# Kernel optimization log

Hardware: AMD Instinct MI355X
Metric: run time of the kernel (lower is better)

The kernel has to match this reference:

```python
import jax, jax.numpy as jnp
import numpy as np

B, P, K, E, H, V, C = 128, 64, 64, 300, 300, 50000, 3


def lstm0(x, Wih, bih, bhh):
    # PyTorch LSTMCell single step with zero initial (h, c) state.
    # gates = x @ Wih^T + bih + Whh @ 0 + bhh ; chunks order: i, f, g, o
    g = x @ Wih.T + bih + bhh
    i, f, gg, o = jnp.split(g, 4, axis=-1)
    c = jax.nn.sigmoid(i) * jnp.tanh(gg)
    return jax.nn.sigmoid(o) * jnp.tanh(c)


def setup_inputs() -> dict:
    key = jax.random.key(0)
    ks = jax.random.split(key, 24)
    d = {}
    d["premise"] = jax.random.randint(ks[0], (B, P), 1, V)
    d["premise_len"] = jax.random.randint(ks[1], (B,), P // 2, P + 1)
    d["hypothesis"] = jax.random.randint(ks[2], (B, K), 1, V)
    d["hypothesis_len"] = jax.random.randint(ks[3], (B,), K // 2, K + 1)
    embed = jax.random.normal(ks[4], (V, E), jnp.float32) * 0.1
    d["embed"] = embed.at[0].set(0.0)  # padding_idx=0
    d["w_e"] = jax.random.uniform(ks[5], (H,), jnp.float32)
    xav = (2.0 / (H + H)) ** 0.5
    d["W_s"] = jax.random.normal(ks[6], (H, H), jnp.float32) * xav
    d["W_t"] = jax.random.normal(ks[7], (H, H), jnp.float32) * xav
    d["W_m"] = jax.random.normal(ks[8], (H, H), jnp.float32) * xav
    d["fc_w"] = jax.random.normal(ks[9], (C, H), jnp.float32) * (2.0 / (H + C)) ** 0.5
    d["fc_b"] = jax.random.uniform(ks[10], (C,), jnp.float32)
    s = 1.0 / np.sqrt(H)
    def cell(k1, k2, k3, k4, in_dim):
        return (jax.random.uniform(k1, (4 * H, in_dim), jnp.float32, -s, s),
                jax.random.uniform(k2, (4 * H, H), jnp.float32, -s, s),
                jax.random.uniform(k3, (4 * H,), jnp.float32, -s, s),
                jax.random.uniform(k4, (4 * H,), jnp.float32, -s, s))
    d["Wih_p"], d["Whh_p"], d["bih_p"], d["bhh_p"] = cell(ks[11], ks[12], ks[13], ks[14], E)
    d["Wih_h"], d["Whh_h"], d["bih_h"], d["bhh_h"] = cell(ks[15], ks[16], ks[17], ks[18], E)
    d["Wih_m"], d["Whh_m"], d["bih_m"], d["bhh_m"] = cell(ks[19], ks[20], ks[21], ks[22], 2 * H)
    return d


def reference(premise, premise_len, hypothesis, hypothesis_len, embed, w_e,
              W_s, W_t, W_m, fc_w, fc_b,
              Wih_p, Whh_p, bih_p, bhh_p,
              Wih_h, Whh_h, bih_h, bhh_h,
              Wih_m, Whh_m, bih_m, bhh_m):
    prem_emb = embed[premise]      # [B,P,E]
    hypo_emb = embed[hypothesis]   # [B,K,E]
    # Original code calls LSTMCell on a whole sequence -> per-token single step
    # with zero initial state (no temporal recurrence in these two cells).
    h_s = lstm0(prem_emb, Wih_p, bih_p, bhh_p)  # [B,P,H]
    h_t = lstm0(hypo_emb, Wih_h, bih_h, bhh_h)  # [B,K,H]
    s_proj = h_s @ W_s.T                         # [B,P,H]
    t_proj = jnp.transpose(h_t @ W_t.T, (1, 0, 2))  # [K,B,H]
    h_t_kb = jnp.transpose(h_t, (1, 0, 2))          # [K,B,H]
    b, p = h_s.shape[0], h_s.shape[1]
    pmask = jnp.arange(p)[None, :] < premise_len[:, None]  # [B,P]
    neg = jnp.finfo(s_proj.dtype).min

    def step(h_m, xs):
        t_k, ht_k = xs  # [B,H], [B,H]
        m_proj = h_m @ W_m.T  # [B,H]
        e = jnp.einsum('bph,h->bp',
                       jnp.tanh(s_proj + t_k[:, None, :] + m_proj[:, None, :]), w_e)
        e = jnp.where(pmask, e, neg)
        alpha = jax.nn.softmax(e, axis=1)           # softmax over valid premise pos
        a = jnp.einsum('bp,bph->bh', alpha, h_s)    # attention-weighted premise
        m = jnp.concatenate([a, ht_k], axis=-1)     # [B,2H]
        # lstm_match is re-invoked with zero state each k in the original
        h_m_new = lstm0(m, Wih_m, bih_m, bhh_m)
        return h_m_new, h_m_new

    _, hs_all = jax.lax.scan(step, jnp.zeros((b, s_proj.shape[-1]), s_proj.dtype),
                             (t_proj, h_t_kb))      # [K,B,H]
    h_fin = hs_all[hypothesis_len - 1, jnp.arange(b)]  # h_m at last valid hypo step
    logits = h_fin @ fc_w.T + fc_b
    return jax.nn.softmax(logits, axis=1)
```

## Files before the change

### kernel.cpp

```cpp
#include <hip/hip_runtime.h>
#include <stdint.h>

typedef unsigned short u16;
typedef __attribute__((ext_vector_type(8))) __bf16 bf16x8;
typedef __attribute__((ext_vector_type(4))) float f32x4;

__device__ __forceinline__ float bf2f(u16 u) {
    union { unsigned int i; float f; } v; v.i = ((unsigned int)u) << 16; return v.f;
}
__device__ __forceinline__ float bf2f_lo(unsigned int u) {
    union { unsigned int i; float f; } v; v.i = u << 16; return v.f;
}
__device__ __forceinline__ float bf2f_hi(unsigned int u) {
    union { unsigned int i; float f; } v; v.i = u & 0xffff0000u; return v.f;
}
__device__ __forceinline__ u16 f2bf(float f) {
    union { float f; unsigned int i; } v; v.f = f;
    unsigned int x = v.i;
    unsigned int r = (x + 0x7fffu + ((x >> 16) & 1u)) >> 16;
    return (u16)r;
}
__device__ __forceinline__ float rdf(const void* p, size_t i, int isbf) {
    return isbf ? bf2f(((const u16*)p)[i]) : ((const float*)p)[i];
}
__device__ __forceinline__ float fast_sigmoid(float x) {
    return __builtin_amdgcn_rcpf(1.f + __expf(-x));
}
__device__ __forceinline__ float fast_tanh(float x) {
    float u = __expf(x + x);
    return 1.f - 2.f * __builtin_amdgcn_rcpf(u + 1.f);
}
__device__ __forceinline__ bf16x8 as_bf8(uint4 u) {
    union { uint4 a; bf16x8 b; } c; c.a = u; return c.b;
}

#define BB 128
#define PP 64
#define KK 64
#define HH 300
#define MROWS 8192
#define KPAD 320
#define N3H 900
#define GLD 912
#define NT1 19
#define NT4 57
#define NW 16

__global__ void detect_dtype(const u16* __restrict__ raw, int* __restrict__ flag) {
    __shared__ int cnt;
    if (threadIdx.x == 0) cnt = 0;
    __syncthreads();
    if (threadIdx.x < 300 && (raw[threadIdx.x] & 0x8000u)) atomicAdd(&cnt, 1);
    __syncthreads();
    if (threadIdx.x == 0) *flag = (cnt < 8) ? 1 : 0;
}

__global__ void pack_w(const void* __restrict__ src, u16* __restrict__ dst,
                       int dstRowsPad, int nsrcRows, int srcld, int colOff, int igo,
                       const int* __restrict__ flag) {
    int i = blockIdx.x * 256 + threadIdx.x;
    if (i >= dstRowsPad * KPAD) return;
    int isbf = *flag;
    int r = i / KPAD, c = i % KPAD;
    u16 v = 0;
    if (r < nsrcRows && c < HH) {
        int sr = igo ? (r < HH ? r : r + HH) : r;
        v = f2bf(rdf(src, (size_t)sr * srcld + colOff + c, isbf));
    }
    dst[i] = v;
}

__global__ void pack_wf(const void* __restrict__ Wm, uint4* __restrict__ dst,
                        const int* __restrict__ flag) {
    int i = blockIdx.x * 256 + threadIdx.x;
    if (i >= NT1 * 10 * 64) return;
    int isbf = *flag;
    int lane = i & 63, ks = (i >> 6) % 10, T = i / 640;
    int j = T * 16 + (lane & 15);
    int k0 = 32 * ks + 8 * (lane >> 4);
    unsigned int d[4];
    #pragma unroll
    for (int q = 0; q < 4; ++q) {
        int ka = k0 + 2 * q, kb = k0 + 2 * q + 1;
        unsigned int lo = (j < 300 && ka < 300) ? f2bf(rdf(Wm, (size_t)j * HH + ka, isbf)) : 0;
        unsigned int hi = (j < 300 && kb < 300) ? f2bf(rdf(Wm, (size_t)j * HH + kb, isbf)) : 0;
        d[q] = lo | (hi << 16);
    }
    uint4 v; v.x = d[0]; v.y = d[1]; v.z = d[2]; v.w = d[3];
    dst[i] = v;
}

__global__ void pack_bias(const void* bip, const void* bhp, const void* bih_, const void* bhh_,
                          const void* bim, const void* bhm,
                          float* bp, float* bh, float* bm, const int* __restrict__ flag) {
    int i = blockIdx.x * 256 + threadIdx.x;
    if (i >= 3 * N3H) return;
    int isbf = *flag;
    int which = i / N3H, r = i % N3H;
    int sr = (r < HH) ? r : r + HH;
    if (which == 0)      bp[r] = rdf(bip, sr, isbf) + rdf(bhp, sr, isbf);
    else if (which == 1) bh[r] = rdf(bih_, sr, isbf) + rdf(bhh_, sr, isbf);
    else                 bm[r] = rdf(bim, sr, isbf) + rdf(bhm, sr, isbf);
}

__global__ void pack_we(const void* __restrict__ we, float* __restrict__ dst,
                        const int* __restrict__ flag) {
    int i = threadIdx.x;
    dst[i] = (i < 300) ? 2.f * rdf(we, i, *flag) : 0.f;
}

__global__ void gather_embed(const int* __restrict__ idx, const void* __restrict__ embed,
                             u16* __restrict__ X, const int* __restrict__ flag) {
    int i = blockIdx.x * 256 + threadIdx.x;
    int isbf = *flag;
    int r = i / KPAD, c = i % KPAD;
    X[i] = (c < HH) ? f2bf(rdf(embed, (size_t)idx[r] * HH + c, isbf)) : (u16)0;
}

__global__ void zero_out(u16* out) { out[threadIdx.x] = 0; }

__global__ __launch_bounds__(256) void gemm_bt(
    const u16* __restrict__ A, const u16* __restrict__ B,
    u16* __restrict__ Cb, const float* __restrict__ bias, int N, int ldc, int frag)
{
    __shared__ __align__(16) u16 At[128 * 32];
    __shared__ __align__(16) u16 Bt[128 * 32];
    const int tid = threadIdx.x;
    const int m0 = blockIdx.x * 128;
    const int n0 = blockIdx.y * 128;
    const int lane = tid & 63;
    const int wave = tid >> 6;
    const int rm = (wave & 1) * 64;
    const int rn = (wave >> 1) * 64;
    const int qr = lane >> 4;
    const int lr = lane & 15;

    f32x4 acc[4][4] = {};

    const int c0 = tid, c1 = tid + 256;
    const int r0 = c0 >> 2, o0 = (c0 & 3) * 8;
    const int r1 = c1 >> 2, o1 = (c1 & 3) * 8;

    for (int k0 = 0; k0 < KPAD; k0 += 32) {
        uint4 a0v = *(const uint4*)(A + (size_t)(m0 + r0) * KPAD + k0 + o0);
        uint4 a1v = *(const uint4*)(A + (size_t)(m0 + r1) * KPAD + k0 + o1);
        uint4 b0v = *(const uint4*)(B + (size_t)(n0 + r0) * KPAD + k0 + o0);
        uint4 b1v = *(const uint4*)(B + (size_t)(n0 + r1) * KPAD + k0 + o1);
        __syncthreads();
        *(uint4*)(At + c0 * 8) = a0v;
        *(uint4*)(At + c1 * 8) = a1v;
        *(uint4*)(Bt + c0 * 8) = b0v;
        *(uint4*)(Bt + c1 * 8) = b1v;
        __syncthreads();
        bf16x8 af[4], bfr[4];
        #pragma unroll
        for (int i = 0; i < 4; ++i) {
            af[i]  = *(const bf16x8*)(At + (rm + i * 16 + lr) * 32 + qr * 8);
            bfr[i] = *(const bf16x8*)(Bt + (rn + i * 16 + lr) * 32 + qr * 8);
        }
        #pragma unroll
        for (int mi = 0; mi < 4; ++mi)
            #pragma unroll
            for (int ni = 0; ni < 4; ++ni)
                acc[mi][ni] = __builtin_amdgcn_mfma_f32_16x16x32_bf16(
                    af[mi], bfr[ni], acc[mi][ni], 0, 0, 0);
    }
    #pragma unroll
    for (int mi = 0; mi < 4; ++mi) {
        #pragma unroll
        for (int ni = 0; ni < 4; ++ni) {
            int n = n0 + rn + ni * 16 + lr;
            int mb = m0 + rm + mi * 16 + qr * 4;
            if (!frag) {
                if (n >= ldc) continue;
                if (n < N) {
                    float bv = bias ? bias[n] : 0.f;
                    #pragma unroll
                    for (int r = 0; r < 4; ++r)
                        Cb[(size_t)(mb + r) * ldc + n] = f2bf(acc[mi][ni][r] + bv);
                } else {
                    #pragma unroll
                    for (int r = 0; r < 4; ++r)
                        Cb[(size_t)(mb + r) * ldc + n] = 0;
                }
            } else {
                if (n >= GLD) continue;
                int bb = mb >> 6, p0 = mb & 63;
                size_t base = ((((size_t)bb * NT4 + (n >> 4)) * 2 + (p0 >> 5)) * 64
                               + ((p0 >> 3) & 3) * 16 + (n & 15)) * 8 + (p0 & 7);
                u16 wv[4];
                if (n < N) {
                    float bv = bias ? bias[n] : 0.f;
                    #pragma unroll
                    for (int r = 0; r < 4; ++r) wv[r] = f2bf(acc[mi][ni][r] + bv);
                } else {
                    #pragma unroll
                    for (int r = 0; r < 4; ++r) wv[r] = 0;
                }
                uint2 st;
                st.x = (unsigned int)wv[0] | ((unsigned int)wv[1] << 16);
                st.y = (unsigned int)wv[2] | ((unsigned int)wv[3] << 16);
                *(uint2*)(Cb + base) = st;
            }
        }
    }
}

__global__ void lstm_act(const u16* __restrict__ gates, u16* __restrict__ hout) {
    int idx = blockIdx.x * 256 + threadIdx.x;
    int r = idx / KPAD, c = idx % KPAD;
    float h = 0.f;
    if (c < HH) {
        const u16* g = gates + (size_t)r * N3H;
        float gi = bf2f(g[c]);
        float gg = bf2f(g[c + HH]);
        float go = bf2f(g[c + 2 * HH]);
        float cc = fast_sigmoid(gi) * fast_tanh(gg);
        h = fast_sigmoid(go) * fast_tanh(cc);
    }
    hout[idx] = f2bf(h);
}

__global__ __launch_bounds__(1024)
__attribute__((amdgpu_waves_per_eu(4, 4)))
void scan_kernel(
    const u16* __restrict__ sproj,
    const u16* __restrict__ tproj,
    const uint4* __restrict__ Gmf,
    const u16* __restrict__ hp,
    const uint4* __restrict__ Wf,
    const float* __restrict__ we2g,
    const int* __restrict__ premise_len,
    const int* __restrict__ hypothesis_len,
    float* __restrict__ hfin)
{
    __shared__ __align__(16) uint4 gml[NT4 * 2 * 64];
    __shared__ __align__(16) uint4 wlds[3 * 10 * 64];
    __shared__ __align__(16) float tpm[320];
    __shared__ __align__(16) unsigned int hmhi[160];
    __shared__ __align__(16) unsigned int hmlo[160];
    __shared__ __align__(16) float part[NW][64];
    __shared__ __align__(16) u16 aw_sh[128];
    __shared__ __align__(16) float gates[912];

    const int b = blockIdx.x, t = threadIdx.x;
    const int lane = t & 63, w = t >> 6;
    const int lr = lane & 15, qr = lane >> 4;
    const int plen = premise_len[b], hlen = hypothesis_len[b];

    {
        const uint4* gsrc = Gmf + (size_t)b * (NT4 * 2 * 64);
        for (int i = t; i < NT4 * 2 * 64; i += 1024) gml[i] = gsrc[i];
    }
    for (int i = t; i < 3 * 10 * 64; i += 1024) wlds[i] = Wf[16 * 640 + i];
    if (t < 320) tpm[t] = 0.f;
    if (t < 160) { hmhi[t] = 0; hmlo[t] = 0; }

    uint4 wreg[10];
    #pragma unroll
    for (int ks = 0; ks < 10; ++ks) wreg[ks] = Wf[(size_t)w * 640 + ks * 64 + lane];

    unsigned int spd[10];
    {
        const u16* srow = sproj + (size_t)(b * PP + lane) * KPAD + 20 * w;
        #pragma unroll
        for (int q = 0; q < 5; ++q) {
            uint2 v = *(const uint2*)(srow + 4 * q);
            spd[2 * q] = v.x; spd[2 * q + 1] = v.y;
        }
    }
    const int wu = __builtin_amdgcn_readfirstlane(w);
    const float* wep = we2g + 20 * wu;
    float we_s[20];
    #pragma unroll
    for (int j = 0; j < 20; ++j) we_s[j] = wep[j];

    float wsumf = 0.f;
    if (w == 0) {
        float s = 0.f;
        #pragma unroll
        for (int q = 0; q < 5; ++q) s += we2g[lane + 64 * q];
        #pragma unroll
        for (int d = 32; d; d >>= 1) s += __shfl_xor(s, d);
        wsumf = 0.5f * s;
    }
    __syncthreads();

    const int nt4 = (w < 9) ? 4 : 3;
    const bool act2 = lane < plen;

    for (int k = 0; k < hlen; ++k) {
        const u16* tprow = tproj + (size_t)(b * KK + k) * KPAD;
        const u16* hprow = hp + (size_t)(b * KK + k) * 900;

        u16 hpv[4];
        #pragma unroll
        for (int i = 0; i < 4; ++i) {
            hpv[i] = 0;
            if (i < nt4 && lane < 16) {
                int j = (w + 16 * i) * 16 + lane;
                if (j < 900) hpv[i] = hprow[j];
            }
        }
        u16 tk0 = 0, tk1 = 0;
        if (lane < 16) {
            tk0 = tprow[w * 16 + lane];
            if (w < 3) tk1 = tprow[(16 + w) * 16 + lane];
        }

        {
            const unsigned int* abase = (lr == 1) ? hmlo : hmhi;
            uint4 z; z.x = 0; z.y = 0; z.z = 0; z.w = 0;
            f32x4 r0 = {}, r1 = {}, l0 = {}, l1 = {};
            #pragma unroll
            for (int h = 0; h < 2; ++h) {
                bf16x8 a1[5];
                #pragma unroll
                for (int j = 0; j < 5; ++j) {
                    int ks = 5 * h + j;
                    uint4 u = *(const uint4*)(abase + 16 * ks + 4 * qr);
                    a1[j] = as_bf8((lr < 2) ? u : z);
                }
                #pragma unroll
                for (int j = 0; j < 5; ++j) {
                    int ks = 5 * h + j;
                    if (j & 1) r1 = __builtin_amdgcn_mfma_f32_16x16x32_bf16(a1[j], as_bf8(wreg[ks]), r1, 0, 0, 0);
                    else       r0 = __builtin_amdgcn_mfma_f32_16x16x32_bf16(a1[j], as_bf8(wreg[ks]), r0, 0, 0, 0);
                }
                if (w < 3) {
                    #pragma unroll
                    for (int j = 0; j < 5; ++j) {
                        int ks = 5 * h + j;
                        bf16x8 bb = as_bf8(wlds[w * 640 + ks * 64 + lane]);
                        if (j & 1) l1 = __builtin_amdgcn_mfma_f32_16x16x32_bf16(a1[j], bb, l1, 0, 0, 0);
                        else       l0 = __builtin_amdgcn_mfma_f32_16x16x32_bf16(a1[j], bb, l0, 0, 0, 0);
                    }
                }
            }
            if (lane < 16) {
                tpm[w * 16 + lane] = 2.f * (bf2f(tk0) + ((r0[0] + r0[1]) + (r1[0] + r1[1])));
                if (w < 3)
                    tpm[(16 + w) * 16 + lane] = 2.f * (bf2f(tk1) + ((l0[0] + l0[1]) + (l1[0] + l1[1])));
            }
        }
        __syncthreads();

        {
            float accn0 = 0.f, accn1 = 0.f;
            if (act2) {
                #pragma unroll
                for (int q = 0; q < 5; ++q) {
                    float4 tv = ((const float4*)tpm)[5 * w + q];
                    float x0 = fmaf(2.f, bf2f_lo(spd[2 * q]), tv.x);
                    float x1 = fmaf(2.f, bf2f_hi(spd[2 * q]), tv.y);
                    float x2 = fmaf(2.f, bf2f_lo(spd[2 * q + 1]), tv.z);
                    float x3 = fmaf(2.f, bf2f_hi(spd[2 * q + 1]), tv.w);
                    accn0 = fmaf(we_s[4 * q],     __builtin_amdgcn_rcpf(__expf(x0) + 1.f), accn0);
                    accn1 = fmaf(we_s[4 * q + 1], __builtin_amdgcn_rcpf(__expf(x1) + 1.f), accn1);
                    accn0 = fmaf(we_s[4 * q + 2], __builtin_amdgcn_rcpf(__expf(x2) + 1.f), accn0);
                    accn1 = fmaf(we_s[4 * q + 3], __builtin_amdgcn_rcpf(__expf(x3) + 1.f), accn1);
                }
            }
            part[w][lane] = act2 ? (accn0 + accn1) : 0.f;
        }
        __syncthreads();

        if (w == 0) {
            float s = 0.f;
            #pragma unroll
            for (int q = 0; q < NW; ++q) s += part[q][lane];
            float e = act2 ? (wsumf - s) : -1e30f;
            float mx = e;
            #pragma unroll
            for (int d = 32; d; d >>= 1) mx = fmaxf(mx, __shfl_xor(mx, d));
            float ex = act2 ? __expf(e - mx) : 0.f;
            float sm = ex;
            #pragma unroll
            for (int d = 32; d; d >>= 1) sm += __shfl_xor(sm, d);
            float al = ex * __builtin_amdgcn_rcpf(sm);
            u16 ah = f2bf(al);
            aw_sh[lane] = ah;
            aw_sh[64 + lane] = f2bf(al - bf2f(ah));
        }
        __syncthreads();

        bf16x8 a4[2];
        {
            const u16* abase = aw_sh + ((lr == 1) ? 64 : 0);
            uint4 z; z.x = 0; z.y = 0; z.z = 0; z.w = 0;
            #pragma unroll
            for (int ks = 0; ks < 2; ++ks) {
                uint4 u = *(const uint4*)(abase + 32 * ks + 8 * qr);
                a4[ks] = as_bf8((lr < 2) ? u : z);
            }
        }
        #pragma unroll
        for (int i = 0; i < 4; ++i) {
            if (i < nt4) {
                int T = w + 16 * i;
                f32x4 ac0 = {}, ac1 = {};
                ac0 = __builtin_amdgcn_mfma_f32_16x16x32_bf16(a4[0], as_bf8(gml[(T * 2 + 0) * 64 + lane]), ac0, 0, 0, 0);
                ac1 = __builtin_amdgcn_mfma_f32_16x16x32_bf16(a4[1], as_bf8(gml[(T * 2 + 1) * 64 + lane]), ac1, 0, 0, 0);
                if (lane < 16) gates[T * 16 + lane] = ((ac0[0] + ac0[1]) + (ac1[0] + ac1[1])) + bf2f(hpv[i]);
            }
        }
        __syncthreads();

        if (t < 300) {
            float gi = gates[t], gg = gates[300 + t], go = gates[600 + t];
            float cc = fast_sigmoid(gi) * fast_tanh(gg);
            float h = fast_sigmoid(go) * fast_tanh(cc);
            if (k == hlen - 1) hfin[(size_t)b * KPAD + t] = h;
            u16 hh = f2bf(h);
            float res = h - bf2f(hh);
            float hn = __shfl_down(h, 1);
            float rn2 = __shfl_down(res, 1);
            if ((t & 1) == 0) {
                hmhi[t >> 1] = (unsigned int)hh | ((unsigned int)f2bf(hn) << 16);
                hmlo[t >> 1] = (unsigned int)f2bf(res) | ((unsigned int)f2bf(rn2) << 16);
            }
        }
        __syncthreads();
    }
}

__global__ void fc_softmax(const float* __restrict__ hfin, const void* __restrict__ fcw,
                           const void* __restrict__ fcb, void* __restrict__ out,
                           const int* __restrict__ flag) {
    int b = threadIdx.x;
    int isbf = *flag;
    float l[3];
    #pragma unroll
    for (int c = 0; c < 3; ++c) {
        float acc = rdf(fcb, c, isbf);
        const float* hr = hfin + (size_t)b * KPAD;
        for (int h = 0; h < HH; ++h) acc += hr[h] * rdf(fcw, (size_t)c * HH + h, isbf);
        l[c] = acc;
    }
    float mx = fmaxf(l[0], fmaxf(l[1], l[2]));
    float e0 = __expf(l[0] - mx), e1 = __expf(l[1] - mx), e2 = __expf(l[2] - mx);
    float inv = __builtin_amdgcn_rcpf(e0 + e1 + e2);
    if (isbf) {
        u16* o = (u16*)out;
        o[b * 3 + 0] = f2bf(e0 * inv);
        o[b * 3 + 1] = f2bf(e1 * inv);
        o[b * 3 + 2] = f2bf(e2 * inv);
    } else {
        float* o = (float*)out;
        o[b * 3 + 0] = e0 * inv;
        o[b * 3 + 1] = e1 * inv;
        o[b * 3 + 2] = e2 * inv;
    }
}

extern "C" void kernel_launch(void* const* d_in, const int* in_sizes, int n_in,
                              void* d_out, int out_size, void* d_ws, size_t ws_size,
                              hipStream_t stream) {
    const int* premise        = (const int*)d_in[0];
    const int* premise_len    = (const int*)d_in[1];
    const int* hypothesis     = (const int*)d_in[2];
    const int* hypothesis_len = (const int*)d_in[3];
    const void* embed = d_in[4];
    const void* w_e   = d_in[5];
    const void* W_s   = d_in[6];
    const void* W_t   = d_in[7];
    const void* W_m   = d_in[8];
    const void* fc_w  = d_in[9];
    const void* fc_b  = d_in[10];
    const void* Wih_p = d_in[11];
    const void* bih_p = d_in[13];
    const void* bhh_p = d_in[14];
    const void* Wih_h = d_in[15];
    const void* bih_h = d_in[17];
    const void* bhh_h = d_in[18];
    const void* Wih_m = d_in[19];
    const void* bih_m = d_in[21];
    const void* bhh_m = d_in[22];
    (void)in_sizes; (void)n_in; (void)out_size;

    char* w = (char*)d_ws;
    auto alloc = [&](size_t bytes) -> char* {
        char* r = (char*)(((uintptr_t)w + 255) & ~(uintptr_t)255);
        w = r + bytes;
        return r;
    };
    char* regA = alloc((size_t)MROWS * KPAD * 2);
    char* regB = alloc((size_t)MROWS * GLD * 2);
    char* regC = alloc((size_t)MROWS * N3H * 2);
    char* regD = alloc((size_t)MROWS * KPAD * 2);
    char* regE = alloc((size_t)MROWS * KPAD * 2);
    u16* Wp_pad  = (u16*)alloc((size_t)1024 * KPAD * 2);
    u16* Wh_pad  = (u16*)alloc((size_t)1024 * KPAD * 2);
    u16* Wa_pad  = (u16*)alloc((size_t)1024 * KPAD * 2);
    u16* Whm_pad = (u16*)alloc((size_t)1024 * KPAD * 2);
    u16* Ws_pad  = (u16*)alloc((size_t)384 * KPAD * 2);
    u16* Wt_pad  = (u16*)alloc((size_t)384 * KPAD * 2);
    uint4* Wf    = (uint4*)alloc((size_t)NT1 * 10 * 64 * 16);
    float* we2g  = (float*)alloc(320 * 4);
    float* bsum_p = (float*)alloc(N3H * 4);
    float* bsum_h = (float*)alloc(N3H * 4);
    float* bsum_m = (float*)alloc(N3H * 4);
    int* dflag   = (int*)alloc(256);
    size_t needed = (size_t)(w - (char*)d_ws);
    if (needed > ws_size) {
        zero_out<<<1, 384, 0, stream>>>((u16*)d_out);
        return;
    }
    u16* Xbuf   = (u16*)regA;
    u16* s_proj = (u16*)regA;
    u16* h_s    = (u16*)regD;
    u16* t_proj = (u16*)regD;
    u16* h_t    = (u16*)regE;
    float* h_fin = (float*)regE;

    detect_dtype<<<1, 320, 0, stream>>>((const u16*)w_e, dflag);
    pack_w<<<1280, 256, 0, stream>>>(Wih_p, Wp_pad, 1024, N3H, HH, 0, 1, dflag);
    pack_w<<<1280, 256, 0, stream>>>(Wih_h, Wh_pad, 1024, N3H, HH, 0, 1, dflag);
    pack_w<<<1280, 256, 0, stream>>>(Wih_m, Wa_pad, 1024, N3H, 600, 0, 1, dflag);
    pack_w<<<1280, 256, 0, stream>>>(Wih_m, Whm_pad, 1024, N3H, 600, HH, 1, dflag);
    pack_w<<<480, 256, 0, stream>>>(W_s, Ws_pad, 384, HH, HH, 0, 0, dflag);
    pack_w<<<480, 256, 0, stream>>>(W_t, Wt_pad, 384, HH, HH, 0, 0, dflag);
    pack_wf<<<48, 256, 0, stream>>>(W_m, Wf, dflag);
    pack_we<<<1, 320, 0, stream>>>(w_e, we2g, dflag);
    pack_bias<<<11, 256, 0, stream>>>(bih_p, bhh_p, bih_h, bhh_h, bih_m, bhh_m,
                                      bsum_p, bsum_h, bsum_m, dflag);

    gather_embed<<<10240, 256, 0, stream>>>(premise, embed, Xbuf, dflag);
    gemm_bt<<<dim3(64, 8), 256, 0, stream>>>(Xbuf, Wp_pad, (u16*)regB, bsum_p, N3H, N3H, 0);
    lstm_act<<<10240, 256, 0, stream>>>((u16*)regB, h_s);
    gather_embed<<<10240, 256, 0, stream>>>(hypothesis, embed, Xbuf, dflag);
    gemm_bt<<<dim3(64, 8), 256, 0, stream>>>(Xbuf, Wh_pad, (u16*)regC, bsum_h, N3H, N3H, 0);
    lstm_act<<<10240, 256, 0, stream>>>((u16*)regC, h_t);

    gemm_bt<<<dim3(64, 3), 256, 0, stream>>>(h_s, Ws_pad, s_proj, nullptr, HH, KPAD, 0);
    gemm_bt<<<dim3(64, 8), 256, 0, stream>>>(h_s, Wa_pad, (u16*)regB, nullptr, N3H, 0, 1);
    gemm_bt<<<dim3(64, 3), 256, 0, stream>>>(h_t, Wt_pad, t_proj, nullptr, HH, KPAD, 0);
    gemm_bt<<<dim3(64, 8), 256, 0, stream>>>(h_t, Whm_pad, (u16*)regC, bsum_m, N3H, N3H, 0);

    scan_kernel<<<BB, 1024, 0, stream>>>(s_proj, t_proj, (const uint4*)regB,
                                         (const u16*)regC, Wf, we2g,
                                         premise_len, hypothesis_len, h_fin);
    fc_softmax<<<1, 128, 0, stream>>>(h_fin, fc_w, fc_b, d_out, dflag);
}
```

Baseline: 623.3 us.

## Broadcast scan projection via readlane, drop LDS barrier, merge pack launches

Inside the scan loop, each wave now keeps its MFMA column result in a register and broadcasts it with readlane. Previously the result went through a shared tpm buffer followed by a __syncthreads. The column ownership of the attention tanh-sum is remapped so each wave handles the same 16 (and optionally 16 more) columns it computed, which removes one block barrier per hypothesis step. Separately, the four gate-weight pack launches are merged into one 2D grid and the final fc_softmax is parallelised across classes. The trade-off is more readlane and SALU work per column plus uneven per-wave work (waves 0-2 do 32 columns, the others 16).

After: 593.7 us. 4.8% less time.

```diff
diff --git a/kernel.cpp b/kernel.cpp
--- a/kernel.cpp
+++ b/kernel.cpp
@@ -32,6 +32,9 @@
 }
 __device__ __forceinline__ bf16x8 as_bf8(uint4 u) {
     union { uint4 a; bf16x8 b; } c; c.a = u; return c.b;
+}
+__device__ __forceinline__ float rdlane_f(float v, int l) {
+    return __int_as_float(__builtin_amdgcn_readlane(__float_as_int(v), l));
 }
 
 #define BB 128
@@ -65,6 +68,28 @@
     u16 v = 0;
     if (r < nsrcRows && c < HH) {
         int sr = igo ? (r < HH ? r : r + HH) : r;
+        v = f2bf(rdf(src, (size_t)sr * srcld + colOff + c, isbf));
+    }
+    dst[i] = v;
+}
+
+__global__ void pack_w_gates(const void* __restrict__ Wp, const void* __restrict__ Wh,
+                             const void* __restrict__ Wm,
+                             u16* __restrict__ dp, u16* __restrict__ dh,
+                             u16* __restrict__ da, u16* __restrict__ dm2,
+                             const int* __restrict__ flag) {
+    int i = blockIdx.x * 256 + threadIdx.x;
+    if (i >= 1024 * KPAD) return;
+    int y = blockIdx.y;
+    int isbf = *flag;
+    const void* src = (y == 0) ? Wp : (y == 1) ? Wh : Wm;
+    u16* dst = (y == 0) ? dp : (y == 1) ? dh : (y == 2) ? da : dm2;
+    int srcld = (y < 2) ? HH : 600;
+    int colOff = (y == 3) ? HH : 0;
+    int r = i / KPAD, c = i % KPAD;
+    u16 v = 0;
+    if (r < N3H && c < HH) {
+        int sr = (r < HH) ? r : r + HH;
         v = f2bf(rdf(src, (size_t)sr * srcld + colOff + c, isbf));
     }
     dst[i] = v;
@@ -221,9 +246,7 @@
     hout[idx] = f2bf(h);
 }
 
-__global__ __launch_bounds__(1024)
-__attribute__((amdgpu_waves_per_eu(4, 4)))
-void scan_kernel(
+__global__ __launch_bounds__(1024, 4) void scan_kernel(
     const u16* __restrict__ sproj,
     const u16* __restrict__ tproj,
     const uint4* __restrict__ Gmf,
@@ -236,7 +259,6 @@
 {
     __shared__ __align__(16) uint4 gml[NT4 * 2 * 64];
     __shared__ __align__(16) uint4 wlds[3 * 10 * 64];
-    __shared__ __align__(16) float tpm[320];
     __shared__ __align__(16) unsigned int hmhi[160];
     __shared__ __align__(16) unsigned int hmlo[160];
     __shared__ __align__(16) float part[NW][64];
@@ -253,27 +275,33 @@
         for (int i = t; i < NT4 * 2 * 64; i += 1024) gml[i] = gsrc[i];
     }
     for (int i = t; i < 3 * 10 * 64; i += 1024) wlds[i] = Wf[16 * 640 + i];
-    if (t < 320) tpm[t] = 0.f;
     if (t < 160) { hmhi[t] = 0; hmlo[t] = 0; }
 
     uint4 wreg[10];
     #pragma unroll
     for (int ks = 0; ks < 10; ++ks) wreg[ks] = Wf[(size_t)w * 640 + ks * 64 + lane];
 
-    unsigned int spd[10];
+    const int wu = __builtin_amdgcn_readfirstlane(w);
+    const bool hasB = (wu < 3);
+    unsigned int spdA[8], spdB[8];
     {
-        const u16* srow = sproj + (size_t)(b * PP + lane) * KPAD + 20 * w;
-        #pragma unroll
-        for (int q = 0; q < 5; ++q) {
-            uint2 v = *(const uint2*)(srow + 4 * q);
-            spd[2 * q] = v.x; spd[2 * q + 1] = v.y;
-        }
-    }
-    const int wu = __builtin_amdgcn_readfirstlane(w);
-    const float* wep = we2g + 20 * wu;
-    float we_s[20];
-    #pragma unroll
-    for (int j = 0; j < 20; ++j) we_s[j] = wep[j];
+        const u16* srow = sproj + (size_t)(b * PP + lane) * KPAD;
+        uint4 v0 = *(const uint4*)(srow + 16 * wu);
+        uint4 v1 = *(const uint4*)(srow + 16 * wu + 8);
+        spdA[0] = v0.x; spdA[1] = v0.y; spdA[2] = v0.z; spdA[3] = v0.w;
+        spdA[4] = v1.x; spdA[5] = v1.y; spdA[6] = v1.z; spdA[7] = v1.w;
+        uint4 v2 = *(const uint4*)(srow + 256 + 16 * wu);
+        uint4 v3 = *(const uint4*)(srow + 256 + 16 * wu + 8);
+        spdB[0] = v2.x; spdB[1] = v2.y; spdB[2] = v2.z; spdB[3] = v2.w;
+        spdB[4] = v3.x; spdB[5] = v3.y; spdB[6] = v3.z; spdB[7] = v3.w;
+    }
+    float weA[16], weB[16];
+    {
+        const float* wA = we2g + 16 * wu;
+        const float* wB = we2g + 256 + 16 * wu;
+        #pragma unroll
+        for (int j = 0; j < 16; ++j) { weA[j] = wA[j]; weB[j] = wB[j]; }
+    }
 
     float wsumf = 0.f;
     if (w == 0) {
@@ -305,9 +333,10 @@
         u16 tk0 = 0, tk1 = 0;
         if (lane < 16) {
             tk0 = tprow[w * 16 + lane];
-            if (w < 3) tk1 = tprow[(16 + w) * 16 + lane];
-        }
-
+            if (hasB) tk1 = tprow[(16 + w) * 16 + lane];
+        }
+
+        float vcolA, vcolB;
         {
             const unsigned int* abase = (lr == 1) ? hmlo : hmhi;
             uint4 z; z.x = 0; z.y = 0; z.z = 0; z.w = 0;
@@ -327,41 +356,41 @@
                     if (j & 1) r1 = __builtin_amdgcn_mfma_f32_16x16x32_bf16(a1[j], as_bf8(wreg[ks]), r1, 0, 0, 0);
                     else       r0 = __builtin_amdgcn_mfma_f32_16x16x32_bf16(a1[j], as_bf8(wreg[ks]), r0, 0, 0, 0);
                 }
-                if (w < 3) {
+                if (hasB) {
                     #pragma unroll
                     for (int j = 0; j < 5; ++j) {
                         int ks = 5 * h + j;
-                        bf16x8 bb = as_bf8(wlds[w * 640 + ks * 64 + lane]);
+                        bf16x8 bb = as_bf8(wlds[wu * 640 + ks * 64 + lane]);
                         if (j & 1) l1 = __builtin_amdgcn_mfma_f32_16x16x32_bf16(a1[j], bb, l1, 0, 0, 0);
                         else       l0 = __builtin_amdgcn_mfma_f32_16x16x32_bf16(a1[j], bb, l0, 0, 0, 0);
                     }
                 }
             }
-            if (lane < 16) {
-                tpm[w * 16 + lane] = 2.f * (bf2f(tk0) + ((r0[0] + r0[1]) + (r1[0] + r1[1])));
-                if (w < 3)
-                    tpm[(16 + w) * 16 + lane] = 2.f * (bf2f(tk1) + ((l0[0] + l0[1]) + (l1[0] + l1[1])));
-            }
-        }
-        __syncthreads();
+            vcolA = 2.f * (bf2f(tk0) + ((r0[0] + r0[1]) + (r1[0] + r1[1])));
+            vcolB = 2.f * (bf2f(tk1) + ((l0[0] + l0[1]) + (l1[0] + l1[1])));
+        }
 
         {
-            float accn0 = 0.f, accn1 = 0.f;
+            float accn = 0.f;
             if (act2) {
                 #pragma unroll
-                for (int q = 0; q < 5; ++q) {
-                    float4 tv = ((const float4*)tpm)[5 * w + q];
-                    float x0 = fmaf(2.f, bf2f_lo(spd[2 * q]), tv.x);
-                    float x1 = fmaf(2.f, bf2f_hi(spd[2 * q]), tv.y);
-                    float x2 = fmaf(2.f, bf2f_lo(spd[2 * q + 1]), tv.z);
-                    float x3 = fmaf(2.f, bf2f_hi(spd[2 * q + 1]), tv.w);
-                    accn0 = fmaf(we_s[4 * q],     __builtin_amdgcn_rcpf(__expf(x0) + 1.f), accn0);
-                    accn1 = fmaf(we_s[4 * q + 1], __builtin_amdgcn_rcpf(__expf(x1) + 1.f), accn1);
-                    accn0 = fmaf(we_s[4 * q + 2], __builtin_amdgcn_rcpf(__expf(x2) + 1.f), accn0);
-                    accn1 = fmaf(we_s[4 * q + 3], __builtin_amdgcn_rcpf(__expf(x3) + 1.f), accn1);
-                }
-            }
-            part[w][lane] = act2 ? (accn0 + accn1) : 0.f;
+                for (int c = 0; c < 16; ++c) {
+                    float xc = rdlane_f(vcolA, c);
+                    float spv = (c & 1) ? bf2f_hi(spdA[c >> 1]) : bf2f_lo(spdA[c >> 1]);
+                    float arg = fmaf(2.f, spv, xc);
+                    accn = fmaf(weA[c], __builtin_amdgcn_rcpf(__expf(arg) + 1.f), accn);
+                }
+                if (hasB) {
+                    #pragma unroll
+                    for (int c = 0; c < 16; ++c) {
+                        float xc = rdlane_f(vcolB, c);
+                        float spv = (c & 1) ? bf2f_hi(spdB[c >> 1]) : bf2f_lo(spdB[c >> 1]);
+                        float arg = fmaf(2.f, spv, xc);
+                        accn = fmaf(weB[c], __builtin_amdgcn_rcpf(__expf(arg) + 1.f), accn);
+                    }
+                }
+            }
+            part[w][lane] = act2 ? accn : 0.f;
         }
         __syncthreads();
 
@@ -427,29 +456,33 @@
 __global__ void fc_softmax(const float* __restrict__ hfin, const void* __restrict__ fcw,
                            const void* __restrict__ fcb, void* __restrict__ out,
                            const int* __restrict__ flag) {
-    int b = threadIdx.x;
+    __shared__ float lg[128][3];
+    int t = threadIdx.x;
+    int b = t & 127, c = t >> 7;
     int isbf = *flag;
-    float l[3];
-    #pragma unroll
-    for (int c = 0; c < 3; ++c) {
+    {
         float acc = rdf(fcb, c, isbf);
         const float* hr = hfin + (size_t)b * KPAD;
         for (int h = 0; h < HH; ++h) acc += hr[h] * rdf(fcw, (size_t)c * HH + h, isbf);
-        l[c] = acc;
-    }
-    float mx = fmaxf(l[0], fmaxf(l[1], l[2]));
-    float e0 = __expf(l[0] - mx), e1 = __expf(l[1] - mx), e2 = __expf(l[2] - mx);
-    float inv = __builtin_amdgcn_rcpf(e0 + e1 + e2);
-    if (isbf) {
-        u16* o = (u16*)out;
-        o[b * 3 + 0] = f2bf(e0 * inv);
-        o[b * 3 + 1] = f2bf(e1 * inv);
-        o[b * 3 + 2] = f2bf(e2 * inv);
-    } else {
-        float* o = (float*)out;
-        o[b * 3 + 0] = e0 * inv;
-        o[b * 3 + 1] = e1 * inv;
-        o[b * 3 + 2] = e2 * inv;
+        lg[b][c] = acc;
+    }
+    __syncthreads();
+    if (t < 128) {
+        float l0 = lg[t][0], l1 = lg[t][1], l2 = lg[t][2];
+        float mx = fmaxf(l0, fmaxf(l1, l2));
+        float e0 = __expf(l0 - mx), e1 = __expf(l1 - mx), e2 = __expf(l2 - mx);
+        float inv = __builtin_amdgcn_rcpf(e0 + e1 + e2);
+        if (isbf) {
+            u16* o = (u16*)out;
+            o[t * 3 + 0] = f2bf(e0 * inv);
+            o[t * 3 + 1] = f2bf(e1 * inv);
+            o[t * 3 + 2] = f2bf(e2 * inv);
+        } else {
+            float* o = (float*)out;
+            o[t * 3 + 0] = e0 * inv;
+            o[t * 3 + 1] = e1 * inv;
+            o[t * 3 + 2] = e2 * inv;
+        }
     }
 }
 
@@ -514,10 +547,8 @@
     float* h_fin = (float*)regE;
 
     detect_dtype<<<1, 320, 0, stream>>>((const u16*)w_e, dflag);
-    pack_w<<<1280, 256, 0, stream>>>(Wih_p, Wp_pad, 1024, N3H, HH, 0, 1, dflag);
-    pack_w<<<1280, 256, 0, stream>>>(Wih_h, Wh_pad, 1024, N3H, HH, 0, 1, dflag);
-    pack_w<<<1280, 256, 0, stream>>>(Wih_m, Wa_pad, 1024, N3H, 600, 0, 1, dflag);
-    pack_w<<<1280, 256, 0, stream>>>(Wih_m, Whm_pad, 1024, N3H, 600, HH, 1, dflag);
+    pack_w_gates<<<dim3(1280, 4), 256, 0, stream>>>(Wih_p, Wih_h, Wih_m,
+                                                    Wp_pad, Wh_pad, Wa_pad, Whm_pad, dflag);
     pack_w<<<480, 256, 0, stream>>>(W_s, Ws_pad, 384, HH, HH, 0, 0, dflag);
     pack_w<<<480, 256, 0, stream>>>(W_t, Wt_pad, 384, HH, HH, 0, 0, dflag);
     pack_wf<<<48, 256, 0, stream>>>(W_m, Wf, dflag);
@@ -540,5 +571,5 @@
     scan_kernel<<<BB, 1024, 0, stream>>>(s_proj, t_proj, (const uint4*)regB,
                                          (const u16*)regC, Wf, we2g,
                                          premise_len, hypothesis_len, h_fin);
-    fc_softmax<<<1, 128, 0, stream>>>(h_fin, fc_w, fc_b, d_out, dflag);
-}
+    fc_softmax<<<1, 384, 0, stream>>>(h_fin, fc_w, fc_b, d_out, dflag);
+}
```
